# Kernel optimization log

Hardware: AMD Instinct MI355X
Metric: run time of the kernel (lower is better)

The kernel has to match this reference:

```python
import jax, jax.numpy as jnp
import numpy as np

N = 50000   # num nodes
C = 256     # in_channels
O = 256     # out_channels
D = 32      # fixed degree per node
S = 16      # num_samples


def setup_inputs() -> dict:
    key = jax.random.key(0)
    ks = jax.random.split(key, 8)
    w = 1.0 / np.sqrt(C).astype(np.float32)
    x = jax.random.normal(ks[0], (N, C), dtype=jnp.float32)
    neighbors = jax.random.randint(ks[1], (N, D), 0, N)  # padded adjacency (degree D for every node)
    W_self = jax.random.uniform(ks[2], (C, O), dtype=jnp.float32, minval=-w, maxval=w)
    b_self = jax.random.uniform(ks[3], (O,), dtype=jnp.float32, minval=-w, maxval=w)
    W_neigh = jax.random.uniform(ks[4], (C, O), dtype=jnp.float32, minval=-w, maxval=w)
    b_neigh = jax.random.uniform(ks[5], (O,), dtype=jnp.float32, minval=-w, maxval=w)
    W_coarsen = jax.random.uniform(ks[6], (C, O), dtype=jnp.float32, minval=-w, maxval=w)
    b_coarsen = jax.random.uniform(ks[7], (O,), dtype=jnp.float32, minval=-w, maxval=w)
    return dict(x=x, W_self=W_self, b_self=b_self, W_neigh=W_neigh, b_neigh=b_neigh,
                W_coarsen=W_coarsen, b_coarsen=b_coarsen, neighbors=neighbors)


def reference(x, W_self, b_self, W_neigh, b_neigh, W_coarsen, b_coarsen, neighbors):
    # Deterministic partition of each node's D neighbors into S sampled + (D-S) unsampled.
    sampled = neighbors[:, :S]     # [N, S]
    unsampled = neighbors[:, S:]   # [N, D-S]
    # Batched gather + mean aggregation (replaces the per-node Python loop).
    agg_s = jnp.mean(x[sampled], axis=1)    # [N, C]
    agg_u = jnp.mean(x[unsampled], axis=1)  # [N, C]
    # out[v] = W_self x[v] + W_neigh mean(sampled) + W_coarsen mean(unsampled) (+ biases)
    out = (x @ W_self + b_self) + (agg_s @ W_neigh + b_neigh) + (agg_u @ W_coarsen + b_coarsen)
    return out
```

## Files before the change

### kernel.cpp

```cpp
#include <hip/hip_runtime.h>
#include <stdint.h>
#include <stddef.h>


#define NN   50000
#define NPAD 50176
#define ODIM 256

typedef __bf16 bf16x8 __attribute__((ext_vector_type(8)));
typedef float  f32x4  __attribute__((ext_vector_type(4)));
typedef float  f32x2  __attribute__((ext_vector_type(2)));
typedef unsigned short u16x8 __attribute__((ext_vector_type(8)));
typedef unsigned short u16x4 __attribute__((ext_vector_type(4)));

static __device__ __forceinline__ unsigned short f2b(float f) {
    unsigned u = __builtin_bit_cast(unsigned, f);
    u += 0x7fffu + ((u >> 16) & 1u);
    return (unsigned short)(u >> 16);
}

__global__ void k_prep_w(const float* __restrict__ Wself, const float* __restrict__ bself,
                         const float* __restrict__ Wneigh, const float* __restrict__ bneigh,
                         const float* __restrict__ Wcoar, const float* __restrict__ bcoar,
                         unsigned short* __restrict__ Wb, float* __restrict__ bias) {
    int k = blockIdx.x;
    int n = threadIdx.x;
    const float* W = (k < 256) ? Wself : (k < 512) ? Wneigh : Wcoar;
    int kl = k & 255;
    float v = W[(size_t)kl * ODIM + n];
    int g = k >> 3;
    int j = k & 7;
    Wb[((size_t)g * ODIM + n) * 8 + j] = f2b(v);
    if (k == 0) bias[n] = bself[n] + bneigh[n] + bcoar[n];
}

__global__ void k_convert_x(const float* __restrict__ x, unsigned short* __restrict__ Ax,
                            unsigned char* __restrict__ X8) {
    int p = blockIdx.x * 256 + threadIdx.x;
    if (p >= NN * 32) return;
    int i  = p >> 5;
    int c8 = p & 31;
    const f32x4* src = (const f32x4*)(x + (size_t)i * 256 + c8 * 8);
    f32x4 v0 = src[0], v1 = src[1];
    u16x8 o;
    o[0] = f2b(v0[0]); o[1] = f2b(v0[1]); o[2] = f2b(v0[2]); o[3] = f2b(v0[3]);
    o[4] = f2b(v1[0]); o[5] = f2b(v1[1]); o[6] = f2b(v1[2]); o[7] = f2b(v1[3]);
    *(u16x8*)(Ax + ((size_t)c8 * NPAD + i) * 8) = o;
    unsigned d0 = __builtin_amdgcn_cvt_pk_fp8_f32(v0[0], v0[1], 0, false);
    d0 = (unsigned)__builtin_amdgcn_cvt_pk_fp8_f32(v0[2], v0[3], d0, true);
    unsigned d1 = __builtin_amdgcn_cvt_pk_fp8_f32(v1[0], v1[1], 0, false);
    d1 = (unsigned)__builtin_amdgcn_cvt_pk_fp8_f32(v1[2], v1[3], d1, true);
    uint2 o8; o8.x = d0; o8.y = d1;
    *(uint2*)(X8 + (size_t)i * 256 + c8 * 8) = o8;
}

__global__ __launch_bounds__(512) void k_gather(const int* __restrict__ nbr,
                                                const unsigned char* __restrict__ X8,
                                                unsigned short* __restrict__ Ax) {
    __shared__ unsigned short aggl[8][512];
    const int wid  = threadIdx.x >> 6;
    const int lane = threadIdx.x & 63;
    const int i = blockIdx.x * 8 + wid;
    const int* nb = nbr + (size_t)i * 32;
    float s0 = 0, s1 = 0, s2 = 0, s3 = 0, u0 = 0, u1 = 0, u2 = 0, u3 = 0;
#pragma unroll
    for (int j = 0; j < 32; ++j) {
        int idx = nb[j];
        unsigned d = *(const unsigned*)(X8 + (size_t)idx * 256 + lane * 4);
        f32x2 lo = __builtin_amdgcn_cvt_pk_f32_fp8(d, false);
        f32x2 hi = __builtin_amdgcn_cvt_pk_f32_fp8(d, true);
        if (j < 16) { s0 += lo[0]; s1 += lo[1]; s2 += hi[0]; s3 += hi[1]; }
        else        { u0 += lo[0]; u1 += lo[1]; u2 += hi[0]; u3 += hi[1]; }
    }
    const float rc = 1.0f / 16.0f;
    u16x4 os = { f2b(s0 * rc), f2b(s1 * rc), f2b(s2 * rc), f2b(s3 * rc) };
    u16x4 ou = { f2b(u0 * rc), f2b(u1 * rc), f2b(u2 * rc), f2b(u3 * rc) };
    *(u16x4*)&aggl[wid][lane * 4]       = os;
    *(u16x4*)&aggl[wid][256 + lane * 4] = ou;
    __syncthreads();
    const int tau = threadIdx.x;
    const int gl = tau >> 3, r = tau & 7;
    u16x8 v = *(const u16x8*)&aggl[r][gl * 8];
    *(u16x8*)(Ax + ((size_t)(32 + gl) * NPAD + blockIdx.x * 8 + r) * 8) = v;
}

#define NT 24

__global__ __launch_bounds__(256, 2) void k_gemm(const unsigned short* __restrict__ Ax,
                                                 const unsigned short* __restrict__ Wb,
                                                 const float* __restrict__ bias,
                                                 float* __restrict__ out) {
    const int tid  = threadIdx.x;
    const int wid  = tid >> 6;
    const int lane = tid & 63;
    const int l15 = lane & 15, l4 = lane >> 4;

    const int bid = blockIdx.x;
    const int g16 = bid >> 4, r16 = bid & 15;
    const int mt = g16 * 8 + (r16 & 7);
    const int nt = r16 >> 3;
    const int row0 = mt * 128;
    const int n0   = nt * 128;
    const int wm = (wid >> 1) * 64, wn = (wid & 1) * 64;

    f32x4 acc[4][4] = {};

    auto loadA = [&](bf16x8* a, int t) {
        const int g = t * 4 + l4;
#pragma unroll
        for (int mi = 0; mi < 4; ++mi)
            a[mi] = *(const bf16x8*)(Ax + ((size_t)g * NPAD + row0 + wm + mi * 16 + l15) * 8);
    };
    auto loadB = [&](bf16x8* b, int t) {
        const int g = t * 4 + l4;
#pragma unroll
        for (int ni = 0; ni < 4; ++ni)
            b[ni] = *(const bf16x8*)(Wb + ((size_t)g * ODIM + n0 + wn + ni * 16 + l15) * 8);
    };

    bf16x8 As[3][4], Bs[3][4];
    loadA(As[0], 0); loadB(Bs[0], 0);
    loadA(As[1], 1); loadB(Bs[1], 1);
#pragma unroll
    for (int t = 0; t < NT; ++t) {
        if (t + 2 < NT) { loadA(As[(t + 2) % 3], t + 2); loadB(Bs[(t + 2) % 3], t + 2); }
        bf16x8* a = As[t % 3];
        bf16x8* b = Bs[t % 3];
#pragma unroll
        for (int mi = 0; mi < 4; ++mi)
#pragma unroll
            for (int ni = 0; ni < 4; ++ni)
                acc[mi][ni] = __builtin_amdgcn_mfma_f32_16x16x32_bf16(
                    a[mi], b[ni], acc[mi][ni], 0, 0, 0);
    }

#pragma unroll
    for (int mi = 0; mi < 4; ++mi) {
        const int row = row0 + wm + mi * 16 + l4 * 4;
#pragma unroll
        for (int ni = 0; ni < 4; ++ni) {
            const int col = n0 + wn + ni * 16 + l15;
            const float bb = bias[col];
            f32x4 v = acc[mi][ni];
#pragma unroll
            for (int r = 0; r < 4; ++r) {
                const int rr = row + r;
                if (rr < NN) out[(size_t)rr * ODIM + col] = v[r] + bb;
            }
        }
    }
}

extern "C" void kernel_launch(void* const* d_in, const int* in_sizes, int n_in,
                              void* d_out, int out_size, void* d_ws, size_t ws_size,
                              hipStream_t stream) {
    const float* x      = (const float*)d_in[0];
    const float* Wself  = (const float*)d_in[1];
    const float* bself  = (const float*)d_in[2];
    const float* Wneigh = (const float*)d_in[3];
    const float* bneigh = (const float*)d_in[4];
    const float* Wcoar  = (const float*)d_in[5];
    const float* bcoar  = (const float*)d_in[6];
    const int*   nbr    = (const int*)d_in[7];
    float* out = (float*)d_out;

    unsigned short* Ax   = (unsigned short*)d_ws;
    unsigned char*  X8   = (unsigned char*)(Ax + (size_t)96 * NPAD * 8);
    unsigned short* Wb   = (unsigned short*)(X8 + (size_t)NN * 256);
    float*          bias = (float*)(Wb + (size_t)96 * ODIM * 8);

    k_prep_w<<<768, 256, 0, stream>>>(Wself, bself, Wneigh, bneigh, Wcoar, bcoar, Wb, bias);
    k_convert_x<<<(NN * 32 + 255) / 256, 256, 0, stream>>>(x, Ax, X8);
    k_gather<<<NN / 8, 512, 0, stream>>>(nbr, X8, Ax);
    k_gemm<<<784, 256, 0, stream>>>(Ax, Wb, bias, out);
}
```

Measured before the change: 109.6 us.

## Transform-then-aggregate: GEMM x against concatenated weights, gather projected rows

Uses linearity to swap the order: x is multiplied once by the concatenated [W_self|W_neigh|W_coarsen] (N=768), which removes the separate bf16/fp8 conversion pass over x. The projected neighbor and coarsen features are stored as fp8, and a final kernel gathers and averages them into the output. The GEMM now reads fp32 x directly and converts to bf16 in registers. It adds byte-granular scattered fp8 stores and a read-modify-write of the output, and the fp8 quantization now applies after projection rather than before.

```diff
diff --git a/kernel.cpp b/kernel.cpp
--- a/kernel.cpp
+++ b/kernel.cpp
@@ -5,13 +5,12 @@
 
 #define NN   50000
 #define NPAD 50176
-#define ODIM 256
+#define CDIM 256
+#define NW   768
 
 typedef __bf16 bf16x8 __attribute__((ext_vector_type(8)));
 typedef float  f32x4  __attribute__((ext_vector_type(4)));
 typedef float  f32x2  __attribute__((ext_vector_type(2)));
-typedef unsigned short u16x8 __attribute__((ext_vector_type(8)));
-typedef unsigned short u16x4 __attribute__((ext_vector_type(4)));
 
 static __device__ __forceinline__ unsigned short f2b(float f) {
     unsigned u = __builtin_bit_cast(unsigned, f);
@@ -25,130 +24,142 @@
                          unsigned short* __restrict__ Wb, float* __restrict__ bias) {
     int k = blockIdx.x;
     int n = threadIdx.x;
-    const float* W = (k < 256) ? Wself : (k < 512) ? Wneigh : Wcoar;
-    int kl = k & 255;
-    float v = W[(size_t)kl * ODIM + n];
-    int g = k >> 3;
-    int j = k & 7;
-    Wb[((size_t)g * ODIM + n) * 8 + j] = f2b(v);
-    if (k == 0) bias[n] = bself[n] + bneigh[n] + bcoar[n];
+    const float* W = (n < 256) ? Wself : (n < 512) ? Wneigh : Wcoar;
+    int nl = n & 255;
+    float v = W[(size_t)k * 256 + nl];
+    int g = k >> 3, j = k & 7;
+    Wb[((size_t)g * NW + n) * 8 + j] = f2b(v);
+    if (k == 0 && n < 256) bias[n] = bself[n] + bneigh[n] + bcoar[n];
 }
 
-__global__ void k_convert_x(const float* __restrict__ x, unsigned short* __restrict__ Ax,
-                            unsigned char* __restrict__ X8) {
-    int p = blockIdx.x * 256 + threadIdx.x;
-    if (p >= NN * 32) return;
-    int i  = p >> 5;
-    int c8 = p & 31;
-    const f32x4* src = (const f32x4*)(x + (size_t)i * 256 + c8 * 8);
-    f32x4 v0 = src[0], v1 = src[1];
-    u16x8 o;
-    o[0] = f2b(v0[0]); o[1] = f2b(v0[1]); o[2] = f2b(v0[2]); o[3] = f2b(v0[3]);
-    o[4] = f2b(v1[0]); o[5] = f2b(v1[1]); o[6] = f2b(v1[2]); o[7] = f2b(v1[3]);
-    *(u16x8*)(Ax + ((size_t)c8 * NPAD + i) * 8) = o;
-    unsigned d0 = __builtin_amdgcn_cvt_pk_fp8_f32(v0[0], v0[1], 0, false);
-    d0 = (unsigned)__builtin_amdgcn_cvt_pk_fp8_f32(v0[2], v0[3], d0, true);
-    unsigned d1 = __builtin_amdgcn_cvt_pk_fp8_f32(v1[0], v1[1], 0, false);
-    d1 = (unsigned)__builtin_amdgcn_cvt_pk_fp8_f32(v1[2], v1[3], d1, true);
-    uint2 o8; o8.x = d0; o8.y = d1;
-    *(uint2*)(X8 + (size_t)i * 256 + c8 * 8) = o8;
-}
-
-__global__ __launch_bounds__(512) void k_gather(const int* __restrict__ nbr,
-                                                const unsigned char* __restrict__ X8,
-                                                unsigned short* __restrict__ Ax) {
-    __shared__ unsigned short aggl[8][512];
-    const int wid  = threadIdx.x >> 6;
-    const int lane = threadIdx.x & 63;
-    const int i = blockIdx.x * 8 + wid;
-    const int* nb = nbr + (size_t)i * 32;
-    float s0 = 0, s1 = 0, s2 = 0, s3 = 0, u0 = 0, u1 = 0, u2 = 0, u3 = 0;
-#pragma unroll
-    for (int j = 0; j < 32; ++j) {
-        int idx = nb[j];
-        unsigned d = *(const unsigned*)(X8 + (size_t)idx * 256 + lane * 4);
-        f32x2 lo = __builtin_amdgcn_cvt_pk_f32_fp8(d, false);
-        f32x2 hi = __builtin_amdgcn_cvt_pk_f32_fp8(d, true);
-        if (j < 16) { s0 += lo[0]; s1 += lo[1]; s2 += hi[0]; s3 += hi[1]; }
-        else        { u0 += lo[0]; u1 += lo[1]; u2 += hi[0]; u3 += hi[1]; }
-    }
-    const float rc = 1.0f / 16.0f;
-    u16x4 os = { f2b(s0 * rc), f2b(s1 * rc), f2b(s2 * rc), f2b(s3 * rc) };
-    u16x4 ou = { f2b(u0 * rc), f2b(u1 * rc), f2b(u2 * rc), f2b(u3 * rc) };
-    *(u16x4*)&aggl[wid][lane * 4]       = os;
-    *(u16x4*)&aggl[wid][256 + lane * 4] = ou;
-    __syncthreads();
-    const int tau = threadIdx.x;
-    const int gl = tau >> 3, r = tau & 7;
-    u16x8 v = *(const u16x8*)&aggl[r][gl * 8];
-    *(u16x8*)(Ax + ((size_t)(32 + gl) * NPAD + blockIdx.x * 8 + r) * 8) = v;
-}
-
-#define NT 24
-
-__global__ __launch_bounds__(256, 2) void k_gemm(const unsigned short* __restrict__ Ax,
+__global__ __launch_bounds__(256, 2) void k_gemm(const float* __restrict__ x,
                                                  const unsigned short* __restrict__ Wb,
                                                  const float* __restrict__ bias,
-                                                 float* __restrict__ out) {
+                                                 float* __restrict__ out,
+                                                 unsigned char* __restrict__ Y8n,
+                                                 unsigned char* __restrict__ Y8c) {
     const int tid  = threadIdx.x;
     const int wid  = tid >> 6;
     const int lane = tid & 63;
     const int l15 = lane & 15, l4 = lane >> 4;
 
     const int bid = blockIdx.x;
-    const int g16 = bid >> 4, r16 = bid & 15;
-    const int mt = g16 * 8 + (r16 & 7);
-    const int nt = r16 >> 3;
+    const int g48 = bid / 48, r48 = bid - g48 * 48;
+    const int mt = g48 * 8 + (r48 & 7);
+    const int nt = r48 >> 3;
     const int row0 = mt * 128;
     const int n0   = nt * 128;
     const int wm = (wid >> 1) * 64, wn = (wid & 1) * 64;
 
-    f32x4 acc[4][4] = {};
+    const float* ap[4];
+#pragma unroll
+    for (int mi = 0; mi < 4; ++mi) {
+        int r = row0 + wm + mi * 16 + l15;
+        if (r > NN - 1) r = NN - 1;
+        ap[mi] = x + (size_t)r * CDIM + l4 * 8;
+    }
 
-    auto loadA = [&](bf16x8* a, int t) {
-        const int g = t * 4 + l4;
+    f32x4  acc[4][4] = {};
+    f32x4  Af[3][4][2];
+    bf16x8 Bs[3][4];
+
+    auto loadA = [&](int s, int t) {
 #pragma unroll
-        for (int mi = 0; mi < 4; ++mi)
-            a[mi] = *(const bf16x8*)(Ax + ((size_t)g * NPAD + row0 + wm + mi * 16 + l15) * 8);
+        for (int mi = 0; mi < 4; ++mi) {
+            Af[s][mi][0] = *(const f32x4*)(ap[mi] + t * 32);
+            Af[s][mi][1] = *(const f32x4*)(ap[mi] + t * 32 + 4);
+        }
     };
-    auto loadB = [&](bf16x8* b, int t) {
+    auto loadB = [&](int s, int t) {
         const int g = t * 4 + l4;
 #pragma unroll
         for (int ni = 0; ni < 4; ++ni)
-            b[ni] = *(const bf16x8*)(Wb + ((size_t)g * ODIM + n0 + wn + ni * 16 + l15) * 8);
+            Bs[s][ni] = *(const bf16x8*)(Wb + ((size_t)g * NW + n0 + wn + ni * 16 + l15) * 8);
     };
-
-    bf16x8 As[3][4], Bs[3][4];
-    loadA(As[0], 0); loadB(Bs[0], 0);
-    loadA(As[1], 1); loadB(Bs[1], 1);
+    auto step = [&](int s) {
 #pragma unroll
-    for (int t = 0; t < NT; ++t) {
-        if (t + 2 < NT) { loadA(As[(t + 2) % 3], t + 2); loadB(Bs[(t + 2) % 3], t + 2); }
-        bf16x8* a = As[t % 3];
-        bf16x8* b = Bs[t % 3];
+        for (int mi = 0; mi < 4; ++mi) {
+            bf16x8 a;
 #pragma unroll
-        for (int mi = 0; mi < 4; ++mi)
+            for (int j = 0; j < 4; ++j) {
+                a[j]     = (__bf16)Af[s][mi][0][j];
+                a[4 + j] = (__bf16)Af[s][mi][1][j];
+            }
 #pragma unroll
             for (int ni = 0; ni < 4; ++ni)
                 acc[mi][ni] = __builtin_amdgcn_mfma_f32_16x16x32_bf16(
-                    a[mi], b[ni], acc[mi][ni], 0, 0, 0);
+                    a, Bs[s][ni], acc[mi][ni], 0, 0, 0);
+        }
+    };
+
+    loadA(0, 0); loadB(0, 0);
+    loadA(1, 1); loadB(1, 1);
+#pragma unroll
+    for (int t = 0; t < 8; ++t) {
+        if (t + 2 < 8) { loadA((t + 2) % 3, t + 2); loadB((t + 2) % 3, t + 2); }
+        step(t % 3);
     }
 
+    if (nt < 2) {
 #pragma unroll
-    for (int mi = 0; mi < 4; ++mi) {
-        const int row = row0 + wm + mi * 16 + l4 * 4;
+        for (int mi = 0; mi < 4; ++mi) {
+            const int row = row0 + wm + mi * 16 + l4 * 4;
 #pragma unroll
-        for (int ni = 0; ni < 4; ++ni) {
-            const int col = n0 + wn + ni * 16 + l15;
-            const float bb = bias[col];
-            f32x4 v = acc[mi][ni];
+            for (int ni = 0; ni < 4; ++ni) {
+                const int col = n0 + wn + ni * 16 + l15;
+                const float bb = bias[col];
+                f32x4 v = acc[mi][ni];
 #pragma unroll
-            for (int r = 0; r < 4; ++r) {
-                const int rr = row + r;
-                if (rr < NN) out[(size_t)rr * ODIM + col] = v[r] + bb;
+                for (int r = 0; r < 4; ++r) {
+                    const int rr = row + r;
+                    if (rr < NN) out[(size_t)rr * 256 + col] = v[r] + bb;
+                }
+            }
+        }
+    } else {
+        unsigned char* G = (nt < 4) ? Y8n : Y8c;
+        const int coff = (nt < 4) ? 256 : 512;
+#pragma unroll
+        for (int mi = 0; mi < 4; ++mi) {
+            const int row = row0 + wm + mi * 16 + l4 * 4;
+#pragma unroll
+            for (int ni = 0; ni < 4; ++ni) {
+                const int col = n0 - coff + wn + ni * 16 + l15;
+                f32x4 v = acc[mi][ni];
+                unsigned w0 = __builtin_amdgcn_cvt_pk_fp8_f32(v[0], v[1], 0, false);
+                unsigned w1 = __builtin_amdgcn_cvt_pk_fp8_f32(v[2], v[3], 0, false);
+                if (row + 0 < NN) G[(size_t)(row + 0) * 256 + col] = (unsigned char)(w0 & 0xff);
+                if (row + 1 < NN) G[(size_t)(row + 1) * 256 + col] = (unsigned char)((w0 >> 8) & 0xff);
+                if (row + 2 < NN) G[(size_t)(row + 2) * 256 + col] = (unsigned char)(w1 & 0xff);
+                if (row + 3 < NN) G[(size_t)(row + 3) * 256 + col] = (unsigned char)((w1 >> 8) & 0xff);
             }
         }
     }
+}
+
+__global__ __launch_bounds__(512) void k_gather_out(const int* __restrict__ nbr,
+                                                    const unsigned char* __restrict__ Y8n,
+                                                    const unsigned char* __restrict__ Y8c,
+                                                    float* __restrict__ out) {
+    const int wid  = threadIdx.x >> 6;
+    const int lane = threadIdx.x & 63;
+    const int i = blockIdx.x * 8 + wid;
+    const int* nb = nbr + (size_t)i * 32;
+    float s0 = 0, s1 = 0, s2 = 0, s3 = 0;
+#pragma unroll
+    for (int j = 0; j < 32; ++j) {
+        const int idx = nb[j];
+        const unsigned char* base = (j < 16) ? Y8n : Y8c;
+        unsigned d = *(const unsigned*)(base + (size_t)idx * 256 + lane * 4);
+        f32x2 lo = __builtin_amdgcn_cvt_pk_f32_fp8(d, false);
+        f32x2 hi = __builtin_amdgcn_cvt_pk_f32_fp8(d, true);
+        s0 += lo[0]; s1 += lo[1]; s2 += hi[0]; s3 += hi[1];
+    }
+    const float rc = 1.0f / 16.0f;
+    f32x4* po = (f32x4*)(out + (size_t)i * 256 + lane * 4);
+    f32x4 o = *po;
+    o[0] += s0 * rc; o[1] += s1 * rc; o[2] += s2 * rc; o[3] += s3 * rc;
+    *po = o;
 }
 
 extern "C" void kernel_launch(void* const* d_in, const int* in_sizes, int n_in,
@@ -164,13 +175,12 @@
     const int*   nbr    = (const int*)d_in[7];
     float* out = (float*)d_out;
 
-    unsigned short* Ax   = (unsigned short*)d_ws;
-    unsigned char*  X8   = (unsigned char*)(Ax + (size_t)96 * NPAD * 8);
-    unsigned short* Wb   = (unsigned short*)(X8 + (size_t)NN * 256);
-    float*          bias = (float*)(Wb + (size_t)96 * ODIM * 8);
+    unsigned short* Wb   = (unsigned short*)d_ws;
+    float*          bias = (float*)(Wb + (size_t)32 * NW * 8);
+    unsigned char*  Y8n  = (unsigned char*)(bias + 256);
+    unsigned char*  Y8c  = Y8n + (size_t)NPAD * 256;
 
-    k_prep_w<<<768, 256, 0, stream>>>(Wself, bself, Wneigh, bneigh, Wcoar, bcoar, Wb, bias);
-    k_convert_x<<<(NN * 32 + 255) / 256, 256, 0, stream>>>(x, Ax, X8);
-    k_gather<<<NN / 8, 512, 0, stream>>>(nbr, X8, Ax);
-    k_gemm<<<784, 256, 0, stream>>>(Ax, Wb, bias, out);
+    k_prep_w<<<256, 768, 0, stream>>>(Wself, bself, Wneigh, bneigh, Wcoar, bcoar, Wb, bias);
+    k_gemm<<<2352, 256, 0, stream>>>(x, Wb, bias, out, Y8n, Y8c);
+    k_gather_out<<<NN / 8, 512, 0, stream>>>(nbr, Y8n, Y8c, out);
 }
```

Measured after the change: 165.3 us. 50.8% more time.
